# Optimization experiments

Measured on AMD Instinct MI355X. Metric: run time of the kernel, lower is better.

Reference implementation:

```python
import jax, jax.numpy as jnp
import numpy as np

B, S, H = 1, 2048, 1024
NH, KVH, HD = 16, 4, 64
E, TOPK, F = 8, 2, 2048
EPS = 1e-5
THETA = 10000.0


def setup_inputs() -> dict:
    key = jax.random.key(0)
    ks = jax.random.split(key, 12)
    s = 0.02
    return {
        "hidden_states": jax.random.normal(ks[0], (B, S, H), jnp.float32),
        "position_ids": jnp.arange(S, dtype=jnp.int64).reshape(1, S),
        "ln1_w": jnp.ones((H,), jnp.float32),
        "ln2_w": jnp.ones((H,), jnp.float32),
        "wq": jax.random.normal(ks[1], (NH * HD, H), jnp.float32) * s,
        "wk": jax.random.normal(ks[2], (KVH * HD, H), jnp.float32) * s,
        "wv": jax.random.normal(ks[3], (KVH * HD, H), jnp.float32) * s,
        "wo": jax.random.normal(ks[4], (H, NH * HD), jnp.float32) * s,
        "gate_w": jax.random.normal(ks[5], (E, H), jnp.float32) * s,
        "w1": jax.random.normal(ks[6], (E, F, H), jnp.float32) * s,
        "w2": jax.random.normal(ks[7], (E, H, F), jnp.float32) * s,
        "w3": jax.random.normal(ks[8], (E, F, H), jnp.float32) * s,
    }


def rmsnorm(x, w, eps=EPS):
    xf = x.astype(jnp.float32)
    v = jnp.mean(xf * xf, axis=-1, keepdims=True)
    return (xf * jax.lax.rsqrt(v + eps)).astype(x.dtype) * w


def rotate_half(x):
    x1, x2 = jnp.split(x, 2, axis=-1)
    return jnp.concatenate([-x2, x1], axis=-1)


def attention(x, position_ids, wq, wk, wv, wo):
    q = (x @ wq.T).reshape(B, S, NH, HD).transpose(0, 2, 1, 3)   # [B,NH,S,HD]
    k = (x @ wk.T).reshape(B, S, KVH, HD).transpose(0, 2, 1, 3)  # [B,KVH,S,HD]
    v = (x @ wv.T).reshape(B, S, KVH, HD).transpose(0, 2, 1, 3)
    inv_freq = 1.0 / (THETA ** (jnp.arange(0, HD, 2, dtype=jnp.float32) / HD))
    ang = position_ids.astype(jnp.float32)[:, :, None] * inv_freq  # [B,S,HD/2]
    emb = jnp.concatenate([ang, ang], axis=-1)                     # [B,S,HD]
    cos = jnp.cos(emb)[:, None]                                    # [B,1,S,HD]
    sin = jnp.sin(emb)[:, None]
    q = q * cos + rotate_half(q) * sin
    k = k * cos + rotate_half(k) * sin
    rep = NH // KVH
    k = jnp.repeat(k, rep, axis=1)
    v = jnp.repeat(v, rep, axis=1)
    scores = jnp.einsum("bhqd,bhkd->bhqk", q, k) / np.sqrt(HD).astype(np.float32)
    causal = jnp.tril(jnp.ones((S, S), bool))
    scores = jnp.where(causal, scores, jnp.finfo(scores.dtype).min)
    attn = jax.nn.softmax(scores, axis=-1)
    ctx = jnp.einsum("bhqk,bhkd->bhqd", attn, v)
    ctx = ctx.transpose(0, 2, 1, 3).reshape(B, S, NH * HD)
    return ctx @ wo.T


def moe(x, gate_w, w1, w2, w3):
    xt = x.reshape(-1, H)                                  # [T,H]
    router_logits = xt @ gate_w.T                          # [T,E]
    probs = jax.nn.softmax(router_logits.astype(jnp.float32), axis=-1)
    topw, topi = jax.lax.top_k(probs, TOPK)                # [T,K]
    topw = topw / jnp.sum(topw, axis=-1, keepdims=True)
    topw = topw.astype(x.dtype)
    # combine weights per expert: [T,E]
    cw = jnp.sum(topw[..., None] * jax.nn.one_hot(topi, E, dtype=x.dtype), axis=1)
    h1 = jnp.einsum("th,efh->etf", xt, w1)
    h3 = jnp.einsum("th,efh->etf", xt, w3)
    g = jax.nn.silu(h1) * h3                               # [E,T,F]
    y = jnp.einsum("etf,ehf->eth", g, w2)                  # [E,T,H]
    out = jnp.einsum("eth,te->th", y, cw)
    return out.reshape(B, S, H), router_logits


def reference(hidden_states, position_ids, ln1_w, ln2_w, wq, wk, wv, wo,
              gate_w, w1, w2, w3):
    residual = hidden_states
    h = rmsnorm(hidden_states, ln1_w)
    h = attention(h, position_ids, wq, wk, wv, wo)
    h = residual + h
    residual = h
    h = rmsnorm(h, ln2_w)
    h, router_logits = moe(h, gate_w, w1, w2, w3)
    h = residual + h
    return h, router_logits
```

## Files before the change

### kernel.cpp

```cpp
#include <hip/hip_runtime.h>
#include <hip/hip_bf16.h>
#include <cstdint>

typedef unsigned short u16;
typedef __attribute__((ext_vector_type(8))) short bh8;
typedef __attribute__((ext_vector_type(4))) short sh4;
typedef __attribute__((ext_vector_type(4))) float fx4;

#define NTOK 2048
#define HDIM 1024
#define NE 8
#define FDIM 2048

#define VMCNT(n) asm volatile("s_waitcnt vmcnt(" #n ")" ::: "memory")
#define LGKM0()  asm volatile("s_waitcnt lgkmcnt(0)" ::: "memory")
#define SBAR()   __builtin_amdgcn_s_barrier()
#define SCB()    __builtin_amdgcn_sched_barrier(0)

__device__ __forceinline__ u16 f2bf(float f) {
    __hip_bfloat16 h = __float2bfloat16(f);
    return __builtin_bit_cast(u16, h);
}

__device__ __forceinline__ void gll16(const void* g, void* l) {
    __builtin_amdgcn_global_load_lds(
        (const __attribute__((address_space(1))) void*)g,
        (__attribute__((address_space(3))) void*)l, 16, 0, 0);
}

__global__ __launch_bounds__(256)
void convert_k(const float* __restrict__ S, u16* __restrict__ D, int n8) {
    int i = blockIdx.x * 256 + threadIdx.x;
    const int stride = gridDim.x * 256;
    for (; i < n8; i += stride) {
        const fx4 a = *(const fx4*)&S[(size_t)i * 8];
        const fx4 b = *(const fx4*)&S[(size_t)i * 8 + 4];
        bh8 o;
        #pragma unroll
        for (int j = 0; j < 4; ++j) {
            o[j]     = (short)f2bf(a[j]);
            o[j + 4] = (short)f2bf(b[j]);
        }
        *(bh8*)&D[(size_t)i * 8] = o;
    }
}

__global__ __launch_bounds__(256)
void rope_table_k(float* __restrict__ cosT, float* __restrict__ sinT) {
    int idx = blockIdx.x * 256 + threadIdx.x;
    int t = idx >> 5, i = idx & 31;
    float freq = powf(10000.0f, -(float)i * (1.0f / 32.0f));
    float ang = (float)t * freq;
    float s, c;
    sincosf(ang, &s, &c);
    cosT[idx] = c;
    sinT[idx] = s;
}

__global__ __launch_bounds__(256)
void rmsnorm_k(const float* __restrict__ X, const float* __restrict__ W, u16* __restrict__ O) {
    const int t = blockIdx.x;
    const int tid = threadIdx.x;
    const fx4 v = *(const fx4*)&X[(size_t)t * HDIM + tid * 4];
    float ss = v[0]*v[0] + v[1]*v[1] + v[2]*v[2] + v[3]*v[3];
    #pragma unroll
    for (int o = 1; o < 64; o <<= 1) ss += __shfl_xor(ss, o);
    __shared__ float red[4];
    if ((tid & 63) == 0) red[tid >> 6] = ss;
    __syncthreads();
    const float inv = rsqrtf((red[0] + red[1] + red[2] + red[3]) * (1.0f / HDIM) + 1e-5f);
    const fx4 w = *(const fx4*)&W[tid * 4];
    sh4 o4;
    #pragma unroll
    for (int i = 0; i < 4; ++i) o4[i] = (short)f2bf(v[i] * inv * w[i]);
    *(sh4*)&O[(size_t)t * HDIM + tid * 4] = o4;
}

__global__ __launch_bounds__(256)
void rmsnorm2_router_k(const float* __restrict__ X, const float* __restrict__ W,
                       const float* __restrict__ GW, u16* __restrict__ O,
                       float* __restrict__ LOGI) {
    const int t = blockIdx.x;
    const int tid = threadIdx.x;
    const fx4 v = *(const fx4*)&X[(size_t)t * HDIM + tid * 4];
    float ss = v[0]*v[0] + v[1]*v[1] + v[2]*v[2] + v[3]*v[3];
    #pragma unroll
    for (int o = 1; o < 64; o <<= 1) ss += __shfl_xor(ss, o);
    __shared__ float red[4];
    if ((tid & 63) == 0) red[tid >> 6] = ss;
    __syncthreads();
    const float inv = rsqrtf((red[0] + red[1] + red[2] + red[3]) * (1.0f / HDIM) + 1e-5f);
    const fx4 w = *(const fx4*)&W[tid * 4];
    fx4 xn;
    #pragma unroll
    for (int i = 0; i < 4; ++i) xn[i] = v[i] * inv * w[i];
    sh4 o4;
    #pragma unroll
    for (int i = 0; i < 4; ++i) o4[i] = (short)f2bf(xn[i]);
    *(sh4*)&O[(size_t)t * HDIM + tid * 4] = o4;

    float part[NE];
    #pragma unroll
    for (int e = 0; e < NE; ++e) {
        const fx4 g = *(const fx4*)&GW[(size_t)e * HDIM + tid * 4];
        part[e] = g[0]*xn[0] + g[1]*xn[1] + g[2]*xn[2] + g[3]*xn[3];
    }
    #pragma unroll
    for (int e = 0; e < NE; ++e)
        #pragma unroll
        for (int o = 1; o < 64; o <<= 1) part[e] += __shfl_xor(part[e], o);
    __shared__ float red8[4][NE];
    if ((tid & 63) == 0) {
        #pragma unroll
        for (int e = 0; e < NE; ++e) red8[tid >> 6][e] = part[e];
    }
    __syncthreads();
    if (tid < NE)
        LOGI[(size_t)t * NE + tid] = red8[0][tid] + red8[1][tid] + red8[2][tid] + red8[3][tid];
}

__global__ __launch_bounds__(256)
void router_topk_k(const float* __restrict__ LOGI, int* __restrict__ counts,
                   int* __restrict__ tokslot, float* __restrict__ wtb) {
    const int t = blockIdx.x * 256 + threadIdx.x;
    float l[NE];
    #pragma unroll
    for (int e = 0; e < NE; ++e) l[e] = LOGI[(size_t)t * NE + e];
    int i0 = 0;
    #pragma unroll
    for (int e = 1; e < NE; ++e) if (l[e] > l[i0]) i0 = e;
    int i1 = (i0 == 0) ? 1 : 0;
    #pragma unroll
    for (int e = 0; e < NE; ++e) if (e != i0 && l[e] > l[i1]) i1 = e;
    float e1 = __expf(l[i1] - l[i0]);
    float w0 = 1.0f / (1.0f + e1);
    float w1 = 1.0f - w0;
    int p0 = atomicAdd(&counts[i0], 1);
    tokslot[i0 * NTOK + p0] = t * 2;
    wtb[i0 * NTOK + p0] = w0;
    int p1 = atomicAdd(&counts[i1], 1);
    tokslot[i1 * NTOK + p1] = t * 2 + 1;
    wtb[i1 * NTOK + p1] = w1;
}

template<int EPI>
__global__ __launch_bounds__(256)
void gemm_bt(const u16* __restrict__ A, const u16* __restrict__ B,
             u16* __restrict__ Cb, float* __restrict__ Cf,
             const int N, const int K,
             const float* __restrict__ aux0, const float* __restrict__ aux1) {
    __shared__ u16 As[2][64 * 32];
    __shared__ u16 Bs[2][64 * 32];

    const int tid = threadIdx.x;
    const int lane = tid & 63;
    const int wid = tid >> 6;
    const int lrow = lane & 15, lgrp = lane >> 4;
    const int wm = wid * 16;
    const int soff = (lgrp ^ ((lrow >> 1) & 3)) * 8;

    const int m0 = blockIdx.y * 64;
    const int n0 = blockIdx.x * 64;

    const int gseg = ((tid & 3) ^ ((tid >> 3) & 3)) * 8;
    const u16* apg = A + (size_t)(m0 + (tid >> 2)) * K + gseg;
    const u16* bpg = B + (size_t)(n0 + (tid >> 2)) * K + gseg;

    fx4 acc[4];
    #pragma unroll
    for (int i = 0; i < 4; ++i) acc[i] = fx4{0.f, 0.f, 0.f, 0.f};

    gll16(apg, &As[0][wid * 512]);
    gll16(bpg, &Bs[0][wid * 512]);

    for (int k0 = 0; k0 < K; k0 += 64) {
        gll16(apg + k0 + 32, &As[1][wid * 512]);
        gll16(bpg + k0 + 32, &Bs[1][wid * 512]);
        VMCNT(2); SBAR(); SCB();
        {
            const bh8 af = *(const bh8*)&As[0][(wm + lrow) * 32 + soff];
            #pragma unroll
            for (int ni = 0; ni < 4; ++ni) {
                const bh8 bf = *(const bh8*)&Bs[0][(ni * 16 + lrow) * 32 + soff];
                acc[ni] = __builtin_amdgcn_mfma_f32_16x16x32_bf16(af, bf, acc[ni], 0, 0, 0);
            }
        }
        LGKM0(); SBAR();
        {
            const int kn = (k0 + 64 < K) ? k0 + 64 : k0;
            gll16(apg + kn, &As[0][wid * 512]);
            gll16(bpg + kn, &Bs[0][wid * 512]);
        }
        VMCNT(2); SBAR(); SCB();
        {
            const bh8 af = *(const bh8*)&As[1][(wm + lrow) * 32 + soff];
            #pragma unroll
            for (int ni = 0; ni < 4; ++ni) {
                const bh8 bf = *(const bh8*)&Bs[1][(ni * 16 + lrow) * 32 + soff];
                acc[ni] = __builtin_amdgcn_mfma_f32_16x16x32_bf16(af, bf, acc[ni], 0, 0, 0);
            }
        }
        LGKM0(); SBAR();
    }
    VMCNT(0);

    #pragma unroll
    for (int j = 0; j < 4; ++j) {
        const int r = m0 + wm + lgrp * 4 + j;
        if (EPI == 3) {
            #pragma unroll
            for (int ni = 0; ni < 2; ++ni) {
                const int d = ni * 16 + lrow;
                const float cv = aux0[r * 32 + d];
                const float sv = aux1[r * 32 + d];
                const float v0 = acc[ni][j];
                const float v1 = acc[ni + 2][j];
                Cb[(size_t)r * N + n0 + d]      = f2bf(v0 * cv - v1 * sv);
                Cb[(size_t)r * N + n0 + d + 32] = f2bf(v1 * cv + v0 * sv);
            }
        } else {
            #pragma unroll
            for (int ni = 0; ni < 4; ++ni) {
                const int c = n0 + ni * 16 + lrow;
                const float v = acc[ni][j];
                if (EPI == 1) Cf[(size_t)r * N + c] = v + aux0[(size_t)r * N + c];
                if (EPI == 2) Cb[(size_t)r * N + c] = f2bf(v);
            }
        }
    }
}

__global__ __launch_bounds__(256)
void attn_part_k(const u16* __restrict__ Q, const u16* __restrict__ Kg,
                 const u16* __restrict__ Vg, float* __restrict__ pacc,
                 float* __restrict__ pl) {
    const int qt = blockIdx.x;
    const int h = blockIdx.y;
    const int c = blockIdx.z;
    if (c * 8 > qt) return;
    const int t0 = c * 8;
    const int tend = min(qt + 1, t0 + 8);
    const int kvh = h >> 2;

    const int tid = threadIdx.x;
    const int lane = tid & 63;
    const int wid = tid >> 6;
    const int lrow = lane & 15, lgrp = lane >> 4;

    __shared__ u16 Ks[64 * 66];
    __shared__ u16 Vs[64 * 66];
    __shared__ u16 Ps[4][16 * 66];

    const int qbase = qt * 64 + wid * 16;

    bh8 qf[2];
    #pragma unroll
    for (int kf = 0; kf < 2; ++kf)
        qf[kf] = *(const bh8*)&Q[(size_t)(qbase + lrow) * 1024 + h * 64 + kf * 32 + lgrp * 8];

    fx4 acc[4];
    #pragma unroll
    for (int ni = 0; ni < 4; ++ni) acc[ni] = fx4{0.f, 0.f, 0.f, 0.f};
    float lsum[4];
    #pragma unroll
    for (int j = 0; j < 4; ++j) lsum[j] = 0.f;

    const int srow = tid >> 2;
    const int sseg = (tid & 3) * 16;

    size_t goff = (size_t)(t0 * 64 + srow) * 256 + kvh * 64 + sseg;
    bh8 kva = *(const bh8*)&Kg[goff];
    bh8 kvb = *(const bh8*)&Kg[goff + 8];
    bh8 vva = *(const bh8*)&Vg[goff];
    bh8 vvb = *(const bh8*)&Vg[goff + 8];

    for (int it = t0; it < tend; ++it) {
        const int kv0 = it * 64;
        __syncthreads();
        *(bh8*)&Ks[srow * 66 + sseg] = kva;
        *(bh8*)&Ks[srow * 66 + sseg + 8] = kvb;
        #pragma unroll
        for (int jj = 0; jj < 8; ++jj) {
            Vs[(sseg + jj) * 66 + srow]     = (u16)vva[jj];
            Vs[(sseg + 8 + jj) * 66 + srow] = (u16)vvb[jj];
        }
        __syncthreads();

        const int itn = (it + 1 < tend) ? it + 1 : it;
        const size_t goff2 = (size_t)(itn * 64 + srow) * 256 + kvh * 64 + sseg;
        kva = *(const bh8*)&Kg[goff2];
        kvb = *(const bh8*)&Kg[goff2 + 8];
        vva = *(const bh8*)&Vg[goff2];
        vvb = *(const bh8*)&Vg[goff2 + 8];

        fx4 s[4];
        #pragma unroll
        for (int nf = 0; nf < 4; ++nf) s[nf] = fx4{0.f, 0.f, 0.f, 0.f};
        #pragma unroll
        for (int kf = 0; kf < 2; ++kf) {
            #pragma unroll
            for (int nf = 0; nf < 4; ++nf) {
                const bh8 kfr = *(const bh8*)&Ks[(nf * 16 + lrow) * 66 + kf * 32 + lgrp * 8];
                s[nf] = __builtin_amdgcn_mfma_f32_16x16x32_bf16(qf[kf], kfr, s[nf], 0, 0, 0);
            }
        }

        #pragma unroll
        for (int nf = 0; nf < 4; ++nf)
            #pragma unroll
            for (int j = 0; j < 4; ++j) {
                const int qr = qbase + lgrp * 4 + j;
                const int kp = kv0 + nf * 16 + lrow;
                float p = __expf(fmaf(s[nf][j], 0.125f, -24.0f));
                p = (kp > qr) ? 0.f : p;
                s[nf][j] = p;
                lsum[j] += p;
            }

        u16* pw = Ps[wid];
        #pragma unroll
        for (int nf = 0; nf < 4; ++nf)
            #pragma unroll
            for (int j = 0; j < 4; ++j)
                pw[(lgrp * 4 + j) * 66 + nf * 16 + lrow] = f2bf(s[nf][j]);

        #pragma unroll
        for (int kf = 0; kf < 2; ++kf) {
            const bh8 pa = *(const bh8*)&pw[lrow * 66 + kf * 32 + lgrp * 8];
            #pragma unroll
            for (int ni = 0; ni < 4; ++ni) {
                const bh8 vb = *(const bh8*)&Vs[(ni * 16 + lrow) * 66 + kf * 32 + lgrp * 8];
                acc[ni] = __builtin_amdgcn_mfma_f32_16x16x32_bf16(pa, vb, acc[ni], 0, 0, 0);
            }
        }
    }

    #pragma unroll
    for (int j = 0; j < 4; ++j) {
        float l = lsum[j];
        #pragma unroll
        for (int o = 1; o < 16; o <<= 1) l += __shfl_xor(l, o);
        lsum[j] = l;
    }

    #pragma unroll
    for (int j = 0; j < 4; ++j) {
        const int r = qbase + lgrp * 4 + j;
        const size_t base = ((size_t)(h * NTOK + r) * 4 + c) * 64;
        #pragma unroll
        for (int ni = 0; ni < 4; ++ni)
            pacc[base + ni * 16 + lrow] = acc[ni][j];
        if (lrow == 0)
            pl[(size_t)(h * NTOK + r) * 4 + c] = lsum[j];
    }
}

__global__ __launch_bounds__(256)
void attn_combine_k(const float* __restrict__ pacc, const float* __restrict__ pl,
                    u16* __restrict__ O) {
    const int idx = blockIdx.x * 4 + (threadIdx.x >> 6);
    const int d = threadIdx.x & 63;
    const int h = idx >> 11;
    const int qrow = idx & 2047;
    const int nch = (qrow >> 9) + 1;

    float den = 0.f, num = 0.f;
    for (int c = 0; c < nch; ++c) {
        den += pl[(size_t)idx * 4 + c];
        num += pacc[((size_t)idx * 4 + c) * 64 + d];
    }
    O[(size_t)qrow * 1024 + h * 64 + d] = f2bf(num / den);
}

__global__ __launch_bounds__(256)
void moe_up_k(const u16* __restrict__ X, const u16* __restrict__ W1b,
              const u16* __restrict__ W3b, const int* __restrict__ counts,
              const int* __restrict__ tokslot, u16* __restrict__ G) {
    const int e = blockIdx.z;
    const int cnt = counts[e];
    const int m0 = blockIdx.y * 64;
    if (m0 >= cnt) return;
    const int n0 = blockIdx.x * 128;

    __shared__ u16 As[2][64 * 32];
    __shared__ u16 B1s[2][128 * 32];
    __shared__ u16 B3s[2][128 * 32];

    const int tid = threadIdx.x;
    const int lane = tid & 63, wid = tid >> 6;
    const int wm = (wid >> 1) * 32, wn = (wid & 1) * 64;
    const int lrow = lane & 15, lgrp = lane >> 4;
    const int soff = (lgrp ^ ((lrow >> 1) & 3)) * 8;

    const int gseg = ((tid & 3) ^ ((tid >> 3) & 3)) * 8;
    const int arow = m0 + (tid >> 2);
    const int tok = (arow < cnt) ? (tokslot[e * NTOK + arow] >> 1) : 0;
    const u16* apg = X + (size_t)tok * HDIM + gseg;
    const size_t eoff = (size_t)e * FDIM * HDIM;
    const u16* b1pg = W1b + eoff + (size_t)(n0 + (tid >> 2)) * HDIM + gseg;
    const u16* b3pg = W3b + eoff + (size_t)(n0 + (tid >> 2)) * HDIM + gseg;
    const size_t rr = (size_t)64 * HDIM;

    fx4 acc1[2][4], acc3[2][4];
    #pragma unroll
    for (int i = 0; i < 2; ++i)
        #pragma unroll
        for (int j = 0; j < 4; ++j) {
            acc1[i][j] = fx4{0.f, 0.f, 0.f, 0.f};
            acc3[i][j] = fx4{0.f, 0.f, 0.f, 0.f};
        }

    gll16(apg, &As[0][wid * 512]);
    gll16(b1pg, &B1s[0][wid * 512]);
    gll16(b1pg + rr, &B1s[0][2048 + wid * 512]);
    gll16(b3pg, &B3s[0][wid * 512]);
    gll16(b3pg + rr, &B3s[0][2048 + wid * 512]);

#define MOE_UP_COMPUTE(BUF)                                                          \
    {                                                                                \
        bh8 af[2], b1f[4], b3f[4];                                                   \
        _Pragma("unroll")                                                            \
        for (int mi = 0; mi < 2; ++mi)                                               \
            af[mi] = *(const bh8*)&As[BUF][(wm + mi * 16 + lrow) * 32 + soff];       \
        _Pragma("unroll")                                                            \
        for (int ni = 0; ni < 4; ++ni) {                                             \
            b1f[ni] = *(const bh8*)&B1s[BUF][(wn + ni * 16 + lrow) * 32 + soff];     \
            b3f[ni] = *(const bh8*)&B3s[BUF][(wn + ni * 16 + lrow) * 32 + soff];     \
        }                                                                            \
        _Pragma("unroll")                                                            \
        for (int mi = 0; mi < 2; ++mi)                                               \
            _Pragma("unroll")                                                        \
            for (int ni = 0; ni < 4; ++ni) {                                         \
                acc1[mi][ni] = __builtin_amdgcn_mfma_f32_16x16x32_bf16(af[mi], b1f[ni], acc1[mi][ni], 0, 0, 0); \
                acc3[mi][ni] = __builtin_amdgcn_mfma_f32_16x16x32_bf16(af[mi], b3f[ni], acc3[mi][ni], 0, 0, 0); \
            }                                                                        \
    }

    for (int k0 = 0; k0 < HDIM; k0 += 64) {
        {
            const int kn = k0 + 32;
            gll16(apg + kn, &As[1][wid * 512]);
            gll16(b1pg + kn, &B1s[1][wid * 512]);
            gll16(b1pg + rr + kn, &B1s[1][2048 + wid * 512]);
            gll16(b3pg + kn, &B3s[1][wid * 512]);
            gll16(b3pg + rr + kn, &B3s[1][2048 + wid * 512]);
        }
        VMCNT(5); SBAR(); SCB();
        MOE_UP_COMPUTE(0)
        LGKM0(); SBAR();
        {
            const int kn = (k0 + 64 < HDIM) ? k0 + 64 : k0;
            gll16(apg + kn, &As[0][wid * 512]);
            gll16(b1pg + kn, &B1s[0][wid * 512]);
            gll16(b1pg + rr + kn, &B1s[0][2048 + wid * 512]);
            gll16(b3pg + kn, &B3s[0][wid * 512]);
            gll16(b3pg + rr + kn, &B3s[0][2048 + wid * 512]);
        }
        VMCNT(5); SBAR(); SCB();
        MOE_UP_COMPUTE(1)
        LGKM0(); SBAR();
    }
    VMCNT(0);
#undef MOE_UP_COMPUTE

    #pragma unroll
    for (int mi = 0; mi < 2; ++mi)
        #pragma unroll
        for (int j = 0; j < 4; ++j) {
            const int r = m0 + wm + mi * 16 + lgrp * 4 + j;
            if (r < cnt) {
                #pragma unroll
                for (int ni = 0; ni < 4; ++ni) {
                    const int c = n0 + wn + ni * 16 + lrow;
                    const float h1 = acc1[mi][ni][j];
                    const float h3 = acc3[mi][ni][j];
                    const float gv = h1 / (1.0f + __expf(-h1)) * h3;
                    G[((size_t)e * NTOK + r) * FDIM + c] = f2bf(gv);
                }
            }
        }
}

__global__ __launch_bounds__(256)
void moe_down_k(const u16* __restrict__ G, const u16* __restrict__ W2b,
                const int* __restrict__ counts, const int* __restrict__ tokslot,
                const float* __restrict__ wtb, float* __restrict__ MO) {
    const int e = blockIdx.z;
    const int cnt = counts[e];
    const int m0 = blockIdx.y * 64;
    if (m0 >= cnt) return;
    const int n0 = blockIdx.x * 64;

    __shared__ u16 As[2][64 * 32];
    __shared__ u16 Bs[2][64 * 32];

    const int tid = threadIdx.x;
    const int lane = tid & 63, wid = tid >> 6;
    const int wm = wid * 16;
    const int lrow = lane & 15, lgrp = lane >> 4;
    const int soff = (lgrp ^ ((lrow >> 1) & 3)) * 8;

    const int gseg = ((tid & 3) ^ ((tid >> 3) & 3)) * 8;
    const u16* apg = G + ((size_t)e * NTOK + m0 + (tid >> 2)) * FDIM + gseg;
    const u16* bpg = W2b + (size_t)e * HDIM * FDIM + (size_t)(n0 + (tid >> 2)) * FDIM + gseg;

    fx4 acc[4];
    #pragma unroll
    for (int i = 0; i < 4; ++i) acc[i] = fx4{0.f, 0.f, 0.f, 0.f};

    gll16(apg, &As[0][wid * 512]);
    gll16(bpg, &Bs[0][wid * 512]);

    for (int k0 = 0; k0 < FDIM; k0 += 64) {
        gll16(apg + k0 + 32, &As[1][wid * 512]);
        gll16(bpg + k0 + 32, &Bs[1][wid * 512]);
        VMCNT(2); SBAR(); SCB();
        {
            const bh8 af = *(const bh8*)&As[0][(wm + lrow) * 32 + soff];
            #pragma unroll
            for (int ni = 0; ni < 4; ++ni) {
                const bh8 bf = *(const bh8*)&Bs[0][(ni * 16 + lrow) * 32 + soff];
                acc[ni] = __builtin_amdgcn_mfma_f32_16x16x32_bf16(af, bf, acc[ni], 0, 0, 0);
            }
        }
        LGKM0(); SBAR();
        {
            const int kn = (k0 + 64 < FDIM) ? k0 + 64 : k0;
            gll16(apg + kn, &As[0][wid * 512]);
            gll16(bpg + kn, &Bs[0][wid * 512]);
        }
        VMCNT(2); SBAR(); SCB();
        {
            const bh8 af = *(const bh8*)&As[1][(wm + lrow) * 32 + soff];
            #pragma unroll
            for (int ni = 0; ni < 4; ++ni) {
                const bh8 bf = *(const bh8*)&Bs[1][(ni * 16 + lrow) * 32 + soff];
                acc[ni] = __builtin_amdgcn_mfma_f32_16x16x32_bf16(af, bf, acc[ni], 0, 0, 0);
            }
        }
        LGKM0(); SBAR();
    }
    VMCNT(0);

    #pragma unroll
    for (int j = 0; j < 4; ++j) {
        const int r = m0 + wm + lgrp * 4 + j;
        if (r < cnt) {
            const int ts = tokslot[e * NTOK + r];
            const float wgt = wtb[e * NTOK + r];
            const int tt = ts >> 1;
            const int sl = ts & 1;
            #pragma unroll
            for (int ni = 0; ni < 4; ++ni) {
                const int c = n0 + ni * 16 + lrow;
                MO[((size_t)sl * NTOK + tt) * HDIM + c] = acc[ni][j] * wgt;
            }
        }
    }
}

__global__ __launch_bounds__(256)
void final_add_k(const float* __restrict__ A, const float* __restrict__ B0,
                 const float* __restrict__ B1, float* __restrict__ O) {
    const size_t i = ((size_t)blockIdx.x * 256 + threadIdx.x) * 4;
    const fx4 a = *(const fx4*)&A[i];
    const fx4 b = *(const fx4*)&B0[i];
    const fx4 c = *(const fx4*)&B1[i];
    fx4 r;
    #pragma unroll
    for (int k = 0; k < 4; ++k) r[k] = a[k] + b[k] + c[k];
    *(fx4*)&O[i] = r;
}

extern "C" void kernel_launch(void* const* d_in, const int* in_sizes, int n_in,
                              void* d_out, int out_size, void* d_ws, size_t ws_size,
                              hipStream_t stream) {
    const float* x   = (const float*)d_in[0];
    const float* ln1 = (const float*)d_in[2];
    const float* ln2 = (const float*)d_in[3];
    const float* wq  = (const float*)d_in[4];
    const float* wk  = (const float*)d_in[5];
    const float* wv  = (const float*)d_in[6];
    const float* wo  = (const float*)d_in[7];
    const float* gw  = (const float*)d_in[8];
    const float* w1  = (const float*)d_in[9];
    const float* w2  = (const float*)d_in[10];
    const float* w3  = (const float*)d_in[11];

    float* out_h = (float*)d_out;
    float* out_logits = out_h + (size_t)NTOK * HDIM;

    uint8_t* wsb = (uint8_t*)d_ws;
    size_t off = 0;
    auto alloc = [&](size_t bytes) -> void* {
        void* ptr = wsb + off;
        off = (off + bytes + 255) & ~(size_t)255;
        return ptr;
    };
    u16*   xn1    = (u16*)alloc((size_t)NTOK * HDIM * 2);
    u16*   qb     = (u16*)alloc((size_t)NTOK * 1024 * 2);
    u16*   kb     = (u16*)alloc((size_t)NTOK * 256 * 2);
    u16*   vb     = (u16*)alloc((size_t)NTOK * 256 * 2);
    u16*   ctxb   = (u16*)alloc((size_t)NTOK * 1024 * 2);
    float* hattn  = (float*)alloc((size_t)NTOK * HDIM * 4);
    u16*   xn2    = (u16*)alloc((size_t)NTOK * HDIM * 2);
    float* cosT   = (float*)alloc((size_t)NTOK * 32 * 4);
    float* sinT   = (float*)alloc((size_t)NTOK * 32 * 4);
    int*   counts = (int*)alloc(NE * 4);
    int*   tokslot= (int*)alloc((size_t)NE * NTOK * 4);
    float* wtb    = (float*)alloc((size_t)NE * NTOK * 4);
    u16*   gbuf   = (u16*)alloc((size_t)NE * NTOK * FDIM * 2);
    float* moeb   = (float*)alloc((size_t)2 * NTOK * HDIM * 4);
    u16*   wqb    = (u16*)alloc((size_t)1024 * HDIM * 2);
    u16*   wkb    = (u16*)alloc((size_t)256 * HDIM * 2);
    u16*   wvb    = (u16*)alloc((size_t)256 * HDIM * 2);
    u16*   wob    = (u16*)alloc((size_t)HDIM * 1024 * 2);
    u16*   w1b    = (u16*)alloc((size_t)NE * FDIM * HDIM * 2);
    u16*   w2b    = (u16*)alloc((size_t)NE * HDIM * FDIM * 2);
    u16*   w3b    = (u16*)alloc((size_t)NE * FDIM * HDIM * 2);

    float* pacc = (float*)gbuf;
    float* pl   = pacc + (size_t)16 * NTOK * 4 * 64;

    hipMemsetAsync(counts, 0, NE * 4, stream);

    convert_k<<<512, 256, 0, stream>>>(wq, wqb, 1024 * HDIM / 8);
    convert_k<<<128, 256, 0, stream>>>(wk, wkb, 256 * HDIM / 8);
    convert_k<<<128, 256, 0, stream>>>(wv, wvb, 256 * HDIM / 8);
    convert_k<<<512, 256, 0, stream>>>(wo, wob, HDIM * 1024 / 8);
    convert_k<<<2048, 256, 0, stream>>>(w1, w1b, NE * FDIM * HDIM / 8);
    convert_k<<<2048, 256, 0, stream>>>(w2, w2b, NE * HDIM * FDIM / 8);
    convert_k<<<2048, 256, 0, stream>>>(w3, w3b, NE * FDIM * HDIM / 8);

    rope_table_k<<<256, 256, 0, stream>>>(cosT, sinT);
    rmsnorm_k<<<NTOK, 256, 0, stream>>>(x, ln1, xn1);
    gemm_bt<3><<<dim3(16, 32), 256, 0, stream>>>(xn1, wqb, qb, nullptr, 1024, HDIM, cosT, sinT);
    gemm_bt<3><<<dim3(4, 32), 256, 0, stream>>>(xn1, wkb, kb, nullptr, 256, HDIM, cosT, sinT);
    gemm_bt<2><<<dim3(4, 32), 256, 0, stream>>>(xn1, wvb, vb, nullptr, 256, HDIM, nullptr, nullptr);
    attn_part_k<<<dim3(32, 16, 4), 256, 0, stream>>>(qb, kb, vb, pacc, pl);
    attn_combine_k<<<8192, 256, 0, stream>>>(pacc, pl, ctxb);
    gemm_bt<1><<<dim3(16, 32), 256, 0, stream>>>(ctxb, wob, nullptr, hattn, 1024, 1024, x, nullptr);
    rmsnorm2_router_k<<<NTOK, 256, 0, stream>>>(hattn, ln2, gw, xn2, out_logits);
    router_topk_k<<<8, 256, 0, stream>>>(out_logits, counts, tokslot, wtb);
    moe_up_k<<<dim3(16, 32, NE), 256, 0, stream>>>(xn2, w1b, w3b, counts, tokslot, gbuf);
    moe_down_k<<<dim3(16, 32, NE), 256, 0, stream>>>(gbuf, w2b, counts, tokslot, wtb, moeb);
    final_add_k<<<NTOK, 256, 0, stream>>>(hattn, moeb, moeb + (size_t)NTOK * HDIM, out_h);
}
```

Baseline: 405.9 us.

## Merge weight conversions into one launch and pre-transpose V for attention

Replaces seven per-weight fp32-to-bf16 conversion launches with a single kernel that walks one contiguous bf16 arena, cutting launch overhead and tail gaps. Adds a small kernel that transposes V once into a [channel, token] layout, so attention blocks can store V tiles to shared memory with vector writes instead of scalar strided transposing writes. The cost is an extra launch plus a V round-trip through global memory, and a per-element branch chain in the conversion loop.

```diff
diff --git a/kernel.cpp b/kernel.cpp
--- a/kernel.cpp
+++ b/kernel.cpp
@@ -28,20 +28,47 @@
         (__attribute__((address_space(3))) void*)l, 16, 0, 0);
 }
 
-__global__ __launch_bounds__(256)
-void convert_k(const float* __restrict__ S, u16* __restrict__ D, int n8) {
+#define N8_WQ 131072
+#define N8_WK 32768
+#define N8_WV 32768
+#define N8_WO 131072
+#define N8_W  2097152
+#define B0q 0
+#define B1k (B0q + N8_WQ)
+#define B2v (B1k + N8_WK)
+#define B3o (B2v + N8_WV)
+#define B4a (B3o + N8_WO)
+#define B5b (B4a + N8_W)
+#define B6c (B5b + N8_W)
+#define N8TOT (B6c + N8_W)
+
+__global__ __launch_bounds__(256)
+void convert_all_k(const float* __restrict__ wq, const float* __restrict__ wk,
+                   const float* __restrict__ wv, const float* __restrict__ wo,
+                   const float* __restrict__ w1, const float* __restrict__ w2,
+                   const float* __restrict__ w3, u16* __restrict__ arena) {
     int i = blockIdx.x * 256 + threadIdx.x;
     const int stride = gridDim.x * 256;
-    for (; i < n8; i += stride) {
-        const fx4 a = *(const fx4*)&S[(size_t)i * 8];
-        const fx4 b = *(const fx4*)&S[(size_t)i * 8 + 4];
+    for (; i < N8TOT; i += stride) {
+        const float* src;
+        int base;
+        if (i < B1k)      { src = wq; base = B0q; }
+        else if (i < B2v) { src = wk; base = B1k; }
+        else if (i < B3o) { src = wv; base = B2v; }
+        else if (i < B4a) { src = wo; base = B3o; }
+        else if (i < B5b) { src = w1; base = B4a; }
+        else if (i < B6c) { src = w2; base = B5b; }
+        else              { src = w3; base = B6c; }
+        const size_t li = (size_t)(i - base) * 8;
+        const fx4 a = *(const fx4*)&src[li];
+        const fx4 b = *(const fx4*)&src[li + 4];
         bh8 o;
         #pragma unroll
         for (int j = 0; j < 4; ++j) {
             o[j]     = (short)f2bf(a[j]);
             o[j + 4] = (short)f2bf(b[j]);
         }
-        *(bh8*)&D[(size_t)i * 8] = o;
+        *(bh8*)&arena[(size_t)i * 8] = o;
     }
 }
 
@@ -231,8 +258,33 @@
 }
 
 __global__ __launch_bounds__(256)
+void transpose_v_k(const u16* __restrict__ V, u16* __restrict__ VT) {
+    __shared__ u16 Ls[64 * 66];
+    const int tid = threadIdx.x;
+    const int c0 = blockIdx.x * 64;
+    const int t0 = blockIdx.y * 64;
+
+    const int r = tid >> 2;
+    const int seg = (tid & 3) * 16;
+    const size_t src = (size_t)(t0 + r) * 256 + c0 + seg;
+    *(bh8*)&Ls[r * 66 + seg]     = *(const bh8*)&V[src];
+    *(bh8*)&Ls[r * 66 + seg + 8] = *(const bh8*)&V[src + 8];
+    __syncthreads();
+    const int c = tid >> 2;
+    bh8 o0, o1;
+    #pragma unroll
+    for (int j = 0; j < 8; ++j) {
+        o0[j] = (short)Ls[(seg + j) * 66 + c];
+        o1[j] = (short)Ls[(seg + 8 + j) * 66 + c];
+    }
+    const size_t dst = (size_t)(c0 + c) * NTOK + t0 + seg;
+    *(bh8*)&VT[dst]     = o0;
+    *(bh8*)&VT[dst + 8] = o1;
+}
+
+__global__ __launch_bounds__(256)
 void attn_part_k(const u16* __restrict__ Q, const u16* __restrict__ Kg,
-                 const u16* __restrict__ Vg, float* __restrict__ pacc,
+                 const u16* __restrict__ VTg, float* __restrict__ pacc,
                  float* __restrict__ pl) {
     const int qt = blockIdx.x;
     const int h = blockIdx.y;
@@ -268,30 +320,29 @@
     const int srow = tid >> 2;
     const int sseg = (tid & 3) * 16;
 
-    size_t goff = (size_t)(t0 * 64 + srow) * 256 + kvh * 64 + sseg;
-    bh8 kva = *(const bh8*)&Kg[goff];
-    bh8 kvb = *(const bh8*)&Kg[goff + 8];
-    bh8 vva = *(const bh8*)&Vg[goff];
-    bh8 vvb = *(const bh8*)&Vg[goff + 8];
+    size_t gk = (size_t)(t0 * 64 + srow) * 256 + kvh * 64 + sseg;
+    size_t gv = (size_t)(kvh * 64 + srow) * NTOK + t0 * 64 + sseg;
+    bh8 kva = *(const bh8*)&Kg[gk];
+    bh8 kvb = *(const bh8*)&Kg[gk + 8];
+    bh8 vva = *(const bh8*)&VTg[gv];
+    bh8 vvb = *(const bh8*)&VTg[gv + 8];
 
     for (int it = t0; it < tend; ++it) {
         const int kv0 = it * 64;
         __syncthreads();
-        *(bh8*)&Ks[srow * 66 + sseg] = kva;
+        *(bh8*)&Ks[srow * 66 + sseg]     = kva;
         *(bh8*)&Ks[srow * 66 + sseg + 8] = kvb;
-        #pragma unroll
-        for (int jj = 0; jj < 8; ++jj) {
-            Vs[(sseg + jj) * 66 + srow]     = (u16)vva[jj];
-            Vs[(sseg + 8 + jj) * 66 + srow] = (u16)vvb[jj];
-        }
+        *(bh8*)&Vs[srow * 66 + sseg]     = vva;
+        *(bh8*)&Vs[srow * 66 + sseg + 8] = vvb;
         __syncthreads();
 
         const int itn = (it + 1 < tend) ? it + 1 : it;
-        const size_t goff2 = (size_t)(itn * 64 + srow) * 256 + kvh * 64 + sseg;
-        kva = *(const bh8*)&Kg[goff2];
-        kvb = *(const bh8*)&Kg[goff2 + 8];
-        vva = *(const bh8*)&Vg[goff2];
-        vvb = *(const bh8*)&Vg[goff2 + 8];
+        const size_t gk2 = (size_t)(itn * 64 + srow) * 256 + kvh * 64 + sseg;
+        const size_t gv2 = (size_t)(kvh * 64 + srow) * NTOK + itn * 64 + sseg;
+        kva = *(const bh8*)&Kg[gk2];
+        kvb = *(const bh8*)&Kg[gk2 + 8];
+        vva = *(const bh8*)&VTg[gv2];
+        vvb = *(const bh8*)&VTg[gv2 + 8];
 
         fx4 s[4];
         #pragma unroll
@@ -601,6 +652,7 @@
     u16*   qb     = (u16*)alloc((size_t)NTOK * 1024 * 2);
     u16*   kb     = (u16*)alloc((size_t)NTOK * 256 * 2);
     u16*   vb     = (u16*)alloc((size_t)NTOK * 256 * 2);
+    u16*   vbt    = (u16*)alloc((size_t)256 * NTOK * 2);
     u16*   ctxb   = (u16*)alloc((size_t)NTOK * 1024 * 2);
     float* hattn  = (float*)alloc((size_t)NTOK * HDIM * 4);
     u16*   xn2    = (u16*)alloc((size_t)NTOK * HDIM * 2);
@@ -611,33 +663,29 @@
     float* wtb    = (float*)alloc((size_t)NE * NTOK * 4);
     u16*   gbuf   = (u16*)alloc((size_t)NE * NTOK * FDIM * 2);
     float* moeb   = (float*)alloc((size_t)2 * NTOK * HDIM * 4);
-    u16*   wqb    = (u16*)alloc((size_t)1024 * HDIM * 2);
-    u16*   wkb    = (u16*)alloc((size_t)256 * HDIM * 2);
-    u16*   wvb    = (u16*)alloc((size_t)256 * HDIM * 2);
-    u16*   wob    = (u16*)alloc((size_t)HDIM * 1024 * 2);
-    u16*   w1b    = (u16*)alloc((size_t)NE * FDIM * HDIM * 2);
-    u16*   w2b    = (u16*)alloc((size_t)NE * HDIM * FDIM * 2);
-    u16*   w3b    = (u16*)alloc((size_t)NE * FDIM * HDIM * 2);
+    u16*   arena  = (u16*)alloc((size_t)N8TOT * 8 * 2);
+    u16*   wqb    = arena;
+    u16*   wkb    = arena + (size_t)B1k * 8;
+    u16*   wvb    = arena + (size_t)B2v * 8;
+    u16*   wob    = arena + (size_t)B3o * 8;
+    u16*   w1b    = arena + (size_t)B4a * 8;
+    u16*   w2b    = arena + (size_t)B5b * 8;
+    u16*   w3b    = arena + (size_t)B6c * 8;
 
     float* pacc = (float*)gbuf;
     float* pl   = pacc + (size_t)16 * NTOK * 4 * 64;
 
     hipMemsetAsync(counts, 0, NE * 4, stream);
 
-    convert_k<<<512, 256, 0, stream>>>(wq, wqb, 1024 * HDIM / 8);
-    convert_k<<<128, 256, 0, stream>>>(wk, wkb, 256 * HDIM / 8);
-    convert_k<<<128, 256, 0, stream>>>(wv, wvb, 256 * HDIM / 8);
-    convert_k<<<512, 256, 0, stream>>>(wo, wob, HDIM * 1024 / 8);
-    convert_k<<<2048, 256, 0, stream>>>(w1, w1b, NE * FDIM * HDIM / 8);
-    convert_k<<<2048, 256, 0, stream>>>(w2, w2b, NE * HDIM * FDIM / 8);
-    convert_k<<<2048, 256, 0, stream>>>(w3, w3b, NE * FDIM * HDIM / 8);
+    convert_all_k<<<2048, 256, 0, stream>>>(wq, wk, wv, wo, w1, w2, w3, arena);
 
     rope_table_k<<<256, 256, 0, stream>>>(cosT, sinT);
     rmsnorm_k<<<NTOK, 256, 0, stream>>>(x, ln1, xn1);
     gemm_bt<3><<<dim3(16, 32), 256, 0, stream>>>(xn1, wqb, qb, nullptr, 1024, HDIM, cosT, sinT);
     gemm_bt<3><<<dim3(4, 32), 256, 0, stream>>>(xn1, wkb, kb, nullptr, 256, HDIM, cosT, sinT);
     gemm_bt<2><<<dim3(4, 32), 256, 0, stream>>>(xn1, wvb, vb, nullptr, 256, HDIM, nullptr, nullptr);
-    attn_part_k<<<dim3(32, 16, 4), 256, 0, stream>>>(qb, kb, vb, pacc, pl);
+    transpose_v_k<<<dim3(4, 32), 256, 0, stream>>>(vb, vbt);
+    attn_part_k<<<dim3(32, 16, 4), 256, 0, stream>>>(qb, kb, vbt, pacc, pl);
     attn_combine_k<<<8192, 256, 0, stream>>>(pacc, pl, ctxb);
     gemm_bt<1><<<dim3(16, 32), 256, 0, stream>>>(ctxb, wob, nullptr, hattn, 1024, 1024, x, nullptr);
     rmsnorm2_router_k<<<NTOK, 256, 0, stream>>>(hattn, ln2, gw, xn2, out_logits);
```

New measurement: 387.5 us. 1.05x faster.
